# Kernel optimization log

Hardware: AMD Instinct MI355X
Metric: run time of the kernel (lower is better)

The kernel has to match this reference:

```python
import jax, jax.numpy as jnp
import numpy as np

P = 512       # person_attrs_dim
Z = 4096      # num_zones
T = 16384     # number of timesteps
E = 65536     # number of edges
PENALTY = 10.0


def setup_inputs() -> dict:
    key = jax.random.key(0)
    ks = jax.random.split(key, 10)
    person_attrs = jax.random.normal(ks[0], (P,), dtype=jnp.float32)
    times = jax.random.uniform(ks[1], (T,), dtype=jnp.float32)
    zone_features = jax.random.normal(ks[2], (Z, 16), dtype=jnp.float32)
    edge_index = jax.random.randint(ks[3], (2, E), 0, Z, dtype=jnp.int64)
    s = 0.05
    W1 = jax.random.normal(ks[4], (P + 1, 128), dtype=jnp.float32) * s
    b1 = jnp.zeros((128,), jnp.float32)
    W2 = jax.random.normal(ks[5], (128, 64), dtype=jnp.float32) * s
    b2 = jnp.zeros((64,), jnp.float32)
    W3 = jax.random.normal(ks[6], (64, Z), dtype=jnp.float32) * s
    b3 = jnp.zeros((Z,), jnp.float32)
    return {
        "person_attrs": person_attrs, "times": times,
        "zone_features": zone_features, "edge_index": edge_index,
        "W1": W1, "b1": b1, "W2": W2, "b2": b2, "W3": W3, "b3": b3,
    }


def reference(person_attrs, times, zone_features, edge_index, W1, b1, W2, b2, W3, b3):
    Zn = W3.shape[1]
    Tn = times.shape[0]

    # ---- set_graph_data: symmetric adjacency + self loops ----
    adj = jnp.zeros((Zn, Zn), jnp.float32)
    adj = adj.at[edge_index[0], edge_index[1]].set(1.0)
    adj = adj.at[edge_index[1], edge_index[0]].set(1.0)
    diag = jnp.arange(Zn)
    adj = adj.at[diag, diag].set(1.0)

    # ---- batched MLP over all timesteps (inputs don't depend on decode state) ----
    # input per step: concat(person_attrs, time)  -> [T, P+1]
    x = jnp.concatenate(
        [jnp.broadcast_to(person_attrs, (Tn, person_attrs.shape[0])), times[:, None]],
        axis=1,
    )
    h = jax.nn.relu(x @ W1 + b1)          # [T, 128]  (dropout is identity in eval)
    h = jax.nn.relu(h @ W2 + b2)          # [T, 64]
    raw = h @ W3 + b3                     # [T, Z]

    # ---- sequential graph-masked decode (training=True soft-penalty branch) ----
    def step(cur_zone, raw_t):
        constrained = raw_t - PENALTY * (1.0 - adj[cur_zone])  # [Z]
        nxt = jnp.argmax(constrained).astype(jnp.int32)
        return nxt, constrained

    _, zone_logits = jax.lax.scan(step, jnp.int32(0), raw)     # [T, Z]
    return zone_logits
```

## Files before the change

kernel.cpp:

```cpp
#include <hip/hip_runtime.h>
#include <hip/hip_bf16.h>
#include <stdint.h>

typedef uint16_t u16;
typedef uint32_t u32;
typedef uint64_t u64;
typedef unsigned char u8;

#define TT 16384
#define ZZ 4096
#define EE 65536
#define LBLK 32
#define NBLK 512
#define SUPW 16
#define NSUP 32
#define ADJ_STRIDE 80
#define UCAP 2048
#define PEN 10.0f

#define WS_BITS   0x000000
#define WS_GMKEY  0x200000
#define WS_DEG    0x220000
#define WS_ADJL   0x224000
#define WS_NCH    0x2C4000
#define WS_CVEC   0x2C5000
#define WS_WVEC   0x2C5200
#define WS_H2     0x2C5400
#define WS_M      WS_H2
#define WS_H      0x6C5400
#define WS_SB     0x705400
#define WS_CUR    0x705C00

__device__ __forceinline__ u32 sfu(float v) {
  u32 u = __float_as_uint(v);
  return u ^ ((u32)((int)u >> 31) | 0x80000000u);
}
__device__ __forceinline__ u64 mkkey(float v, u32 z) {
  return ((u64)sfu(v) << 12) | (u64)(4095u - z);
}
__device__ __forceinline__ float key_val(u64 k) {
  u32 sf = (u32)(k >> 12);
  u32 u = (sf & 0x80000000u) ? (sf ^ 0x80000000u) : ~sf;
  return __uint_as_float(u);
}

__device__ __forceinline__ u64 eval_part(int s, int part, const u32* keys, u64 gkey,
                                         const u16* adjl, int nc) {
  const u64* alq = (const u64*)(adjl + (size_t)s * ADJ_STRIDE);
  u64 c0 = (part      < nc) ? alq[part]      : 0;
  u64 c1 = (part + 4  < nc) ? alq[part + 4]  : 0;
  u64 c2 = (part + 8  < nc) ? alq[part + 8]  : 0;
  u64 c3 = (part + 12 < nc) ? alq[part + 12] : 0;
  u64 c4 = (part + 16 < nc) ? alq[part + 16] : 0;
  u64 bb = gkey;
#define CM(cv, cnd) if (cnd) {                                                   \
    u32 lo = (u32)(cv), hi = (u32)((cv) >> 32);                                  \
    u32 za = lo & 0xFFFFu, zb = lo >> 16, zc = hi & 0xFFFFu, zd = hi >> 16;      \
    u64 k0 = ((u64)keys[za] << 32) | (u64)(za ^ 0xFFFu);                         \
    u64 k1 = ((u64)keys[zb] << 32) | (u64)(zb ^ 0xFFFu);                         \
    u64 k2 = ((u64)keys[zc] << 32) | (u64)(zc ^ 0xFFFu);                         \
    u64 k3 = ((u64)keys[zd] << 32) | (u64)(zd ^ 0xFFFu);                         \
    u64 t01 = k0 > k1 ? k0 : k1; u64 t23 = k2 > k3 ? k2 : k3;                    \
    u64 tm = t01 > t23 ? t01 : t23;                                              \
    bb = tm > bb ? tm : bb; }
  CM(c0, part < nc) CM(c1, part + 4 < nc) CM(c2, part + 8 < nc)
  CM(c3, part + 12 < nc) CM(c4, part + 16 < nc)
#undef CM
  return bb;
}

__global__ __launch_bounds__(256) void k_setupA(u32* bits, u32* deg, u16* adjl,
                                                const float* pa, const float* W1,
                                                const float* b1,
                                                float* cvec, float* wvec) {
  __shared__ float pal[512];
  int tid = threadIdx.x;
  if (blockIdx.x < 16) {
    int z = blockIdx.x * 256 + tid;
    bits[(size_t)z * 128 + (z >> 5)] = 1u << (z & 31);
    deg[z] = 1;
    adjl[(size_t)z * ADJ_STRIDE] = (u16)z;
    return;
  }
  for (int i = tid; i < 512; i += 256) pal[i] = pa[i];
  __syncthreads();
  if (tid < 128) {
    float acc = b1[tid];
    for (int i = 0; i < 512; i++) acc = fmaf(pal[i], W1[(size_t)i * 128 + tid], acc);
    cvec[tid] = acc;
    wvec[tid] = W1[512 * 128 + tid];
  }
}

__global__ void k_edges(const int* ei, u32* bits, u32* deg, u16* adjl) {
  int e = blockIdx.x * blockDim.x + threadIdx.x;
  if (e >= EE) return;
  int u = ei[e], v = ei[EE + e];
#pragma unroll
  for (int dir = 0; dir < 2; dir++) {
    int a = dir ? v : u, b = dir ? u : v;
    u32 bit = 1u << (b & 31);
    u32 old = atomicOr(&bits[(size_t)a * 128 + (b >> 5)], bit);
    if (!(old & bit)) {
      u32 p = atomicAdd(&deg[a], 1u);
      if (p < ADJ_STRIDE) adjl[(size_t)a * ADJ_STRIDE + p] = (u16)b;
    }
  }
}

__global__ __launch_bounds__(256) void k_setupC(const u32* deg, u16* adjl, u8* nchp,
                                                const float* times, const float* W2,
                                                const float* b2, const float* cvec,
                                                const float* wvec, float* h2) {
  __shared__ float W2T[64][132];
  __shared__ float h1b[4][128];
  __shared__ float cl[128], wl[128], b2l[64];
  int tid = threadIdx.x;
  if (blockIdx.x < 16) {
    int z = blockIdx.x * 256 + tid;
    int d = (int)deg[z]; if (d > ADJ_STRIDE) d = ADJ_STRIDE;
    int dp = (d + 3) & ~3;
    for (int k = d; k < dp; k++) adjl[(size_t)z * ADJ_STRIDE + k] = (u16)z;
    nchp[z] = (u8)(dp >> 2);
    return;
  }
  for (int idx = tid; idx < 128 * 64; idx += 256) {
    int i = idx >> 6, j = idx & 63;
    W2T[j][i] = W2[idx];
  }
  if (tid < 128) { cl[tid] = cvec[tid]; wl[tid] = wvec[tid]; }
  else if (tid < 192) b2l[tid - 128] = b2[tid - 128];
  __syncthreads();
  int w = tid >> 6, lane = tid & 63;
  int t = (blockIdx.x - 16) * 4 + w;
  float tv = times[t];
  h1b[w][lane]      = fmaxf(fmaf(tv, wl[lane],      cl[lane]),      0.f);
  h1b[w][lane + 64] = fmaxf(fmaf(tv, wl[lane + 64], cl[lane + 64]), 0.f);
  __syncthreads();
  float acc = b2l[lane];
  const float4* hr = (const float4*)&h1b[w][0];
  const float4* Wr = (const float4*)&W2T[lane][0];
#pragma unroll
  for (int i4 = 0; i4 < 32; i4++) {
    float4 a = hr[i4], bb = Wr[i4];
    acc += a.x * bb.x; acc += a.y * bb.y; acc += a.z * bb.z; acc += a.w * bb.w;
  }
  acc = fmaxf(acc, 0.f);
  h2[(size_t)t * 64 + lane] = acc;
}

__global__ __launch_bounds__(512) void k_raw(const float* h2, const float* W3,
                                             const float* b3, float* out,
                                             u64* gmkey) {
  __shared__ float w3t[64][128];
  __shared__ float h2t[64][72];
  int tid = threadIdx.x;
  int zblk = blockIdx.x & 31, tblk = blockIdx.x >> 5;
  int z0 = zblk * 128, t0 = tblk * 64;
#pragma unroll
  for (int it = 0; it < 4; it++) {
    int f4 = tid + it * 512;
    int k = f4 >> 5, jj = (f4 & 31) * 4;
    *(float4*)&w3t[k][jj] = *(const float4*)(W3 + (size_t)k * ZZ + z0 + jj);
  }
#pragma unroll
  for (int it = 0; it < 2; it++) {
    int f4 = tid + it * 512;
    int r = f4 >> 4, kk = (f4 & 15) * 4;
    float4 h = *(const float4*)(h2 + (size_t)(t0 + r) * 64 + kk);
    h2t[kk + 0][r] = h.x; h2t[kk + 1][r] = h.y;
    h2t[kk + 2][r] = h.z; h2t[kk + 3][r] = h.w;
  }
  __syncthreads();
  int zq = tid & 31, tq = tid >> 5;
  float4 acc[4];
#pragma unroll
  for (int r = 0; r < 4; r++) acc[r] = make_float4(0.f, 0.f, 0.f, 0.f);
  for (int k = 0; k < 64; k++) {
    float4 w = *(const float4*)&w3t[k][zq * 4];
    float4 h = *(const float4*)&h2t[k][tq * 4];
    acc[0].x += h.x * w.x; acc[0].y += h.x * w.y; acc[0].z += h.x * w.z; acc[0].w += h.x * w.w;
    acc[1].x += h.y * w.x; acc[1].y += h.y * w.y; acc[1].z += h.y * w.z; acc[1].w += h.y * w.w;
    acc[2].x += h.z * w.x; acc[2].y += h.z * w.y; acc[2].z += h.z * w.z; acc[2].w += h.z * w.w;
    acc[3].x += h.w * w.x; acc[3].y += h.w * w.y; acc[3].z += h.w * w.z; acc[3].w += h.w * w.w;
  }
  int z = z0 + zq * 4;
  float4 b3v = *(const float4*)(b3 + z);
  int lane = tid & 63;
  int half = lane >> 5;
#pragma unroll
  for (int r = 0; r < 4; r++) {
    int t = t0 + tq * 4 + r;
    float4 v;
    v.x = acc[r].x + b3v.x - PEN; v.y = acc[r].y + b3v.y - PEN;
    v.z = acc[r].z + b3v.z - PEN; v.w = acc[r].w + b3v.w - PEN;
    *(float4*)(out + (size_t)t * ZZ + z) = v;
    float lv = v.x; u32 lz = (u32)z;
    if (v.y > lv) { lv = v.y; lz = (u32)(z + 1); }
    if (v.z > lv) { lv = v.z; lz = (u32)(z + 2); }
    if (v.w > lv) { lv = v.w; lz = (u32)(z + 3); }
    float mv = lv;
#pragma unroll
    for (int off = 16; off >= 1; off >>= 1) {
      float o = __shfl_xor(mv, off);
      mv = o > mv ? o : mv;
    }
    u64 msk = __ballot(lv == mv);
    u32 hm = (u32)(msk >> (half * 32));
    int fl = __ffs(hm) - 1 + half * 32;
    u32 zbest = __shfl(lz, fl);
    if ((lane & 31) == 0)
      atomicMax((unsigned long long*)&gmkey[t], (unsigned long long)mkkey(mv, zbest));
  }
}

__global__ __launch_bounds__(512) void k_stage1(const float* raw, const u16* adjl,
                                                const u8* nchp, const u64* gmkey,
                                                u16* M) {
  __shared__ u32 keys[ZZ];
  __shared__ u16 ev0[ZZ];
  __shared__ u16 ev[ZZ];
  __shared__ u16 R[ZZ];
  __shared__ u16 U0[UCAP];
  __shared__ u16 U[2][UCAP];
  __shared__ u8  nchl[ZZ];
  __shared__ u32 markw[128];
  __shared__ u32 mcnt2[2];
  __shared__ u64 gmk[LBLK];
  int tid = threadIdx.x;
  int b = blockIdx.x, t0 = b * LBLK;
  *(u64*)&nchl[tid * 8] = *(const u64*)(nchp + tid * 8);
  if (tid < LBLK) gmk[tid] = gmkey[t0 + tid];
  {
    const float4* src = (const float4*)(raw + (size_t)t0 * ZZ);
    float4 r0 = src[tid], r1 = src[tid + 512];
    ((uint4*)keys)[tid]       = make_uint4(sfu(r0.x), sfu(r0.y), sfu(r0.z), sfu(r0.w));
    ((uint4*)keys)[tid + 512] = make_uint4(sfu(r1.x), sfu(r1.y), sfu(r1.z), sfu(r1.w));
  }
  if (tid < 128) markw[tid] = 0;
  if (tid == 128) { mcnt2[0] = 0; mcnt2[1] = 0; }
  __syncthreads();
  int lane = tid & 63;
  u64 lmask = (((u64)1) << lane) - 1ull;
  int part = tid & 3;
  {
    const float4* srcn = (const float4*)(raw + (size_t)(t0 + 1) * ZZ);
    float4 p0 = srcn[tid], p1 = srcn[tid + 512];
    u64 gk = gmk[0];
    float gv = key_val(gk) - PEN;
    u64 gkey = ((u64)sfu(gv) << 32) | (u64)(gk & 0xFFFu);
    for (int u = tid; u < ZZ * 4; u += 512) {
      int s = u >> 2;
      u64 pk = eval_part(s, part, keys, gkey, adjl, (int)nchl[s]);
      u64 o1 = __shfl_xor(pk, 1); pk = o1 > pk ? o1 : pk;
      u64 o2 = __shfl_xor(pk, 2); pk = o2 > pk ? o2 : pk;
      if (part == 0) ev0[s] = (u16)(4095u - ((u32)pk & 0xFFFu));
    }
    __syncthreads();
    for (int ch = 0; ch < 8; ch++) {
      u32 ns = ev0[ch * 512 + tid];
      u32 wi = ns >> 5, bit = 1u << (ns & 31);
      u32 old = atomicOr(&markw[wi], bit);
      bool isnew = !(old & bit);
      u64 msk = __ballot(isnew ? 1 : 0);
      u32 base = 0;
      if (lane == 0) base = msk ? atomicAdd(&mcnt2[0], (u32)__popcll(msk)) : 0u;
      base = __shfl(base, 0);
      if (isnew) {
        u32 idx = base + (u32)__popcll(msk & lmask);
        if (idx < UCAP) { U[0][idx] = (u16)ns; U0[idx] = (u16)ns; }
        R[ns] = (u16)ns;
      }
    }
    ((uint4*)keys)[tid]       = make_uint4(sfu(p0.x), sfu(p0.y), sfu(p0.z), sfu(p0.w));
    ((uint4*)keys)[tid + 512] = make_uint4(sfu(p1.x), sfu(p1.y), sfu(p1.z), sfu(p1.w));
    __syncthreads();
  }
  int m0r = (int)mcnt2[0];
  bool full0 = (m0r > UCAP);
  int m0 = full0 ? ZZ : m0r;
  if (full0) {
#pragma unroll
    for (int q = 0; q < 8; q++) {
      int j = tid + q * 512;
      R[j] = (u16)j;
    }
    __syncthreads();
  }
  int m = m0;
  bool dense = full0;
  int pb = 0;
  for (int i = 1; i < LBLK; i++) {
    int t = t0 + i;
    int tn = t + 1; if (tn > TT - 1) tn = TT - 1;
    const float4* srcn = (const float4*)(raw + (size_t)tn * ZZ);
    float4 p0 = srcn[tid], p1 = srcn[tid + 512];
    if (tid < 128) markw[tid] = 0;
    if (tid == 128) mcnt2[pb ^ 1] = 0;
    u64 gk = gmk[i];
    float gv = key_val(gk) - PEN;
    u64 gkey = ((u64)sfu(gv) << 32) | (u64)(gk & 0xFFFu);
    int m4 = m << 2;
    for (int u = tid; u < m4; u += 512) {
      int s = dense ? (u >> 2) : (int)U[pb][u >> 2];
      u64 pk = eval_part(s, part, keys, gkey, adjl, (int)nchl[s]);
      u64 o1 = __shfl_xor(pk, 1); pk = o1 > pk ? o1 : pk;
      u64 o2 = __shfl_xor(pk, 2); pk = o2 > pk ? o2 : pk;
      if (part == 0) ev[s] = (u16)(4095u - ((u32)pk & 0xFFFu));
    }
    __syncthreads();
    for (int u = tid; u < m0; u += 512) {
      int v = full0 ? u : (int)U0[u];
      R[v] = ev[R[v]];
    }
    for (int u = tid; u < m; u += 512) {
      int s = dense ? u : (int)U[pb][u];
      u32 ns = ev[s];
      u32 wi = ns >> 5, bit = 1u << (ns & 31);
      u32 old = atomicOr(&markw[wi], bit);
      bool isnew = !(old & bit);
      u64 msk = __ballot(isnew ? 1 : 0);
      u32 base = 0;
      if (lane == 0) base = msk ? atomicAdd(&mcnt2[pb ^ 1], (u32)__popcll(msk)) : 0u;
      base = __shfl(base, 0);
      if (isnew) {
        u32 idx = base + (u32)__popcll(msk & lmask);
        if (idx < UCAP) U[pb ^ 1][idx] = (u16)ns;
      }
    }
    ((uint4*)keys)[tid]       = make_uint4(sfu(p0.x), sfu(p0.y), sfu(p0.z), sfu(p0.w));
    ((uint4*)keys)[tid + 512] = make_uint4(sfu(p1.x), sfu(p1.y), sfu(p1.z), sfu(p1.w));
    __syncthreads();
    m = (int)mcnt2[pb ^ 1];
    dense = (m > UCAP);
    if (dense) m = ZZ;
    pb ^= 1;
  }
  {
    int j0 = tid * 8;
    u64 w0 = (u64)R[ev0[j0 + 0]]
           | ((u64)R[ev0[j0 + 1]] << 16)
           | ((u64)R[ev0[j0 + 2]] << 32)
           | ((u64)R[ev0[j0 + 3]] << 48);
    u64 w1 = (u64)R[ev0[j0 + 4]]
           | ((u64)R[ev0[j0 + 5]] << 16)
           | ((u64)R[ev0[j0 + 6]] << 32)
           | ((u64)R[ev0[j0 + 7]] << 48);
    u64* md = (u64*)(M + (size_t)b * ZZ);
    md[tid * 2]     = w0;
    md[tid * 2 + 1] = w1;
  }
}

__global__ __launch_bounds__(256) void k_super(const u16* G, u16* H) {
  int g = blockIdx.x, tid = threadIdx.x;
  u32 v[16];
#pragma unroll
  for (int q = 0; q < 16; q++) v[q] = G[(size_t)(g * SUPW) * ZZ + tid + q * 256];
  for (int k = 1; k < SUPW; k++) {
    const u16* Gk = G + (size_t)(g * SUPW + k) * ZZ;
#pragma unroll
    for (int q = 0; q < 16; q++) v[q] = Gk[v[q]];
  }
#pragma unroll
  for (int q = 0; q < 16; q++) H[(size_t)g * ZZ + tid + q * 256] = (u16)v[q];
}

__global__ void k_chase(const u16* G, const u16* H, u32* sb) {
  __shared__ u32 ug[NSUP];
  int tid = threadIdx.x;
  if (tid == 0) {
    u32 s = 0;
    for (int g = 0; g < NSUP; g++) { ug[g] = s; s = H[(size_t)g * ZZ + s]; }
  }
  __syncthreads();
  if (tid < NSUP) {
    u32 s = ug[tid];
    for (int k = 0; k < SUPW; k++) {
      int b = tid * SUPW + k;
      sb[b] = s;
      s = G[(size_t)b * ZZ + s];
    }
  }
}

__global__ __launch_bounds__(64) void k_replay2(const float* out, const u16* adjl,
                                                const u8* nchp, const u64* gmkey,
                                                const u32* sb, u32* curz) {
  int b = blockIdx.x, t0 = b * LBLK;
  int lane = threadIdx.x;
  u32 s = sb[b];
  for (int i = 0; i < LBLK; i++) {
    int t = t0 + i;
    if (lane == 0) curz[t] = s;
    u64 gk = gmkey[t];
    float gv = key_val(gk) - PEN;
    u32 gi = 4095u - (u32)(gk & 0xFFFu);
    int dp = ((int)nchp[s]) << 2;
    const u16* al = adjl + (size_t)s * ADJ_STRIDE;
    const float* r = out + (size_t)t * ZZ;
    float bv = gv; u32 bi = gi;
    if (lane < dp) {
      u32 nb = al[lane]; float v = r[nb];
      if (v > bv || (v == bv && nb < bi)) { bv = v; bi = nb; }
    }
    if (lane + 64 < dp) {
      u32 nb = al[lane + 64]; float v = r[nb];
      if (v > bv || (v == bv && nb < bi)) { bv = v; bi = nb; }
    }
#pragma unroll
    for (int off = 32; off >= 1; off >>= 1) {
      float ov = __shfl_xor(bv, off);
      u32 oi  = __shfl_xor(bi, off);
      if (ov > bv || (ov == bv && oi < bi)) { bv = ov; bi = oi; }
    }
    s = bi;
  }
}

__global__ __launch_bounds__(256) void k_out2(float* out, const u32* curz, const u32* bits) {
  int t = blockIdx.x * 4 + (threadIdx.x >> 6);
  int lane = threadIdx.x & 63;
  u32 c = curz[t];
  u64 w = ((const u64*)(bits + (size_t)c * 128))[lane];
  float* p = out + (size_t)t * ZZ + lane * 64;
  while (w) {
    int bpos = __ffsll((unsigned long long)w) - 1;
    p[bpos] += PEN;
    w &= w - 1;
  }
}

extern "C" void kernel_launch(void* const* d_in, const int* in_sizes, int n_in,
                              void* d_out, int out_size, void* d_ws, size_t ws_size,
                              hipStream_t stream) {
  const float* pa    = (const float*)d_in[0];
  const float* times = (const float*)d_in[1];
  const int*   ei    = (const int*)d_in[3];
  const float* W1    = (const float*)d_in[4];
  const float* b1    = (const float*)d_in[5];
  const float* W2    = (const float*)d_in[6];
  const float* b2    = (const float*)d_in[7];
  const float* W3    = (const float*)d_in[8];
  const float* b3    = (const float*)d_in[9];
  float* out = (float*)d_out;
  char* ws = (char*)d_ws;

  u32* bits = (u32*)(ws + WS_BITS);
  u64* gmkey = (u64*)(ws + WS_GMKEY);
  u32* deg  = (u32*)(ws + WS_DEG);
  u16* adjl = (u16*)(ws + WS_ADJL);
  u8*  nchp = (u8*)(ws + WS_NCH);
  float* cvec = (float*)(ws + WS_CVEC);
  float* wvec = (float*)(ws + WS_WVEC);
  float* h2   = (float*)(ws + WS_H2);
  u16* M = (u16*)(ws + WS_M);
  u16* H = (u16*)(ws + WS_H);
  u32* sb   = (u32*)(ws + WS_SB);
  u32* curz = (u32*)(ws + WS_CUR);

  hipMemsetAsync(ws, 0, 0x220000, stream);
  hipLaunchKernelGGL(k_setupA, dim3(17), dim3(256), 0, stream,
                     bits, deg, adjl, pa, W1, b1, cvec, wvec);
  hipLaunchKernelGGL(k_edges, dim3(EE / 256), dim3(256), 0, stream, ei, bits, deg, adjl);
  hipLaunchKernelGGL(k_setupC, dim3(16 + TT / 4), dim3(256), 0, stream,
                     deg, adjl, nchp, times, W2, b2, cvec, wvec, h2);
  hipLaunchKernelGGL(k_raw, dim3(8192), dim3(512), 0, stream, h2, W3, b3, out, gmkey);
  hipLaunchKernelGGL(k_stage1, dim3(NBLK), dim3(512), 0, stream, out, adjl, nchp, gmkey, M);
  hipLaunchKernelGGL(k_super, dim3(NSUP), dim3(256), 0, stream, M, H);
  hipLaunchKernelGGL(k_chase, dim3(1), dim3(64), 0, stream, M, H, sb);
  hipLaunchKernelGGL(k_replay2, dim3(NBLK), dim3(64), 0, stream, out, adjl, nchp, gmkey, sb, curz);
  hipLaunchKernelGGL(k_out2, dim3(TT / 4), dim3(256), 0, stream, out, curz, bits);
}
```

Measured before the change: 411.1 us.

## Track per-source paths instead of dedup frontier in stage1 decode composition

The sparse path of stage1 drops the per-step frontier deduplication (atomicOr marks, ballot compaction, double-buffered U lists). It instead advances each of the m0 initial unique states independently through all 32 steps, writing results in place in S. Keys are double-buffered, so each step needs one barrier instead of two. The dense fallback recomputes all states and composes R each step. This removes atomics and barriers but forgoes merging paths that converge, and UCAP is halved so the dense fallback triggers more often.

```diff
diff --git a/kernel.cpp b/kernel.cpp
--- a/kernel.cpp
+++ b/kernel.cpp
@@ -15,7 +15,7 @@
 #define SUPW 16
 #define NSUP 32
 #define ADJ_STRIDE 80
-#define UCAP 2048
+#define UCAP 1024
 #define PEN 10.0f
 
 #define WS_BITS   0x000000
@@ -217,15 +217,15 @@
 __global__ __launch_bounds__(512) void k_stage1(const float* raw, const u16* adjl,
                                                 const u8* nchp, const u64* gmkey,
                                                 u16* M) {
-  __shared__ u32 keys[ZZ];
+  __shared__ u32 keys[2][ZZ];
   __shared__ u16 ev0[ZZ];
-  __shared__ u16 ev[ZZ];
   __shared__ u16 R[ZZ];
+  __shared__ u16 evf[ZZ];
   __shared__ u16 U0[UCAP];
-  __shared__ u16 U[2][UCAP];
+  __shared__ u16 S[UCAP];
   __shared__ u8  nchl[ZZ];
   __shared__ u32 markw[128];
-  __shared__ u32 mcnt2[2];
+  __shared__ u32 mcnt;
   __shared__ u64 gmk[LBLK];
   int tid = threadIdx.x;
   int b = blockIdx.x, t0 = b * LBLK;
@@ -234,11 +234,11 @@
   {
     const float4* src = (const float4*)(raw + (size_t)t0 * ZZ);
     float4 r0 = src[tid], r1 = src[tid + 512];
-    ((uint4*)keys)[tid]       = make_uint4(sfu(r0.x), sfu(r0.y), sfu(r0.z), sfu(r0.w));
-    ((uint4*)keys)[tid + 512] = make_uint4(sfu(r1.x), sfu(r1.y), sfu(r1.z), sfu(r1.w));
+    ((uint4*)keys[0])[tid]       = make_uint4(sfu(r0.x), sfu(r0.y), sfu(r0.z), sfu(r0.w));
+    ((uint4*)keys[0])[tid + 512] = make_uint4(sfu(r1.x), sfu(r1.y), sfu(r1.z), sfu(r1.w));
   }
   if (tid < 128) markw[tid] = 0;
-  if (tid == 128) { mcnt2[0] = 0; mcnt2[1] = 0; }
+  if (tid == 128) mcnt = 0;
   __syncthreads();
   int lane = tid & 63;
   u64 lmask = (((u64)1) << lane) - 1ull;
@@ -251,7 +251,7 @@
     u64 gkey = ((u64)sfu(gv) << 32) | (u64)(gk & 0xFFFu);
     for (int u = tid; u < ZZ * 4; u += 512) {
       int s = u >> 2;
-      u64 pk = eval_part(s, part, keys, gkey, adjl, (int)nchl[s]);
+      u64 pk = eval_part(s, part, keys[0], gkey, adjl, (int)nchl[s]);
       u64 o1 = __shfl_xor(pk, 1); pk = o1 > pk ? o1 : pk;
       u64 o2 = __shfl_xor(pk, 2); pk = o2 > pk ? o2 : pk;
       if (part == 0) ev0[s] = (u16)(4095u - ((u32)pk & 0xFFFu));
@@ -264,77 +264,71 @@
       bool isnew = !(old & bit);
       u64 msk = __ballot(isnew ? 1 : 0);
       u32 base = 0;
-      if (lane == 0) base = msk ? atomicAdd(&mcnt2[0], (u32)__popcll(msk)) : 0u;
+      if (lane == 0) base = msk ? atomicAdd(&mcnt, (u32)__popcll(msk)) : 0u;
       base = __shfl(base, 0);
       if (isnew) {
         u32 idx = base + (u32)__popcll(msk & lmask);
-        if (idx < UCAP) { U[0][idx] = (u16)ns; U0[idx] = (u16)ns; }
-        R[ns] = (u16)ns;
+        if (idx < UCAP) { U0[idx] = (u16)ns; S[idx] = (u16)ns; }
       }
     }
-    ((uint4*)keys)[tid]       = make_uint4(sfu(p0.x), sfu(p0.y), sfu(p0.z), sfu(p0.w));
-    ((uint4*)keys)[tid + 512] = make_uint4(sfu(p1.x), sfu(p1.y), sfu(p1.z), sfu(p1.w));
+    ((uint4*)keys[1])[tid]       = make_uint4(sfu(p0.x), sfu(p0.y), sfu(p0.z), sfu(p0.w));
+    ((uint4*)keys[1])[tid + 512] = make_uint4(sfu(p1.x), sfu(p1.y), sfu(p1.z), sfu(p1.w));
     __syncthreads();
   }
-  int m0r = (int)mcnt2[0];
-  bool full0 = (m0r > UCAP);
-  int m0 = full0 ? ZZ : m0r;
-  if (full0) {
-#pragma unroll
-    for (int q = 0; q < 8; q++) {
-      int j = tid + q * 512;
-      R[j] = (u16)j;
-    }
+  int m0 = (int)mcnt;
+  int cur = 1;
+  if (m0 <= UCAP) {
+    for (int i = 1; i < LBLK; i++) {
+      int tn = t0 + i + 1; if (tn > TT - 1) tn = TT - 1;
+      const float4* srcn = (const float4*)(raw + (size_t)tn * ZZ);
+      float4 p0 = srcn[tid], p1 = srcn[tid + 512];
+      u64 gk = gmk[i];
+      float gv = key_val(gk) - PEN;
+      u64 gkey = ((u64)sfu(gv) << 32) | (u64)(gk & 0xFFFu);
+      const u32* kc = keys[cur];
+      for (int u = tid >> 2; u < m0; u += 128) {
+        int s = (int)S[u];
+        u64 pk = eval_part(s, part, kc, gkey, adjl, (int)nchl[s]);
+        u64 o1 = __shfl_xor(pk, 1); pk = o1 > pk ? o1 : pk;
+        u64 o2 = __shfl_xor(pk, 2); pk = o2 > pk ? o2 : pk;
+        if (part == 0) S[u] = (u16)(4095u - ((u32)pk & 0xFFFu));
+      }
+      u32* kn = keys[cur ^ 1];
+      ((uint4*)kn)[tid]       = make_uint4(sfu(p0.x), sfu(p0.y), sfu(p0.z), sfu(p0.w));
+      ((uint4*)kn)[tid + 512] = make_uint4(sfu(p1.x), sfu(p1.y), sfu(p1.z), sfu(p1.w));
+      __syncthreads();
+      cur ^= 1;
+    }
+    for (int u = tid; u < m0; u += 512) R[U0[u]] = S[u];
     __syncthreads();
-  }
-  int m = m0;
-  bool dense = full0;
-  int pb = 0;
-  for (int i = 1; i < LBLK; i++) {
-    int t = t0 + i;
-    int tn = t + 1; if (tn > TT - 1) tn = TT - 1;
-    const float4* srcn = (const float4*)(raw + (size_t)tn * ZZ);
-    float4 p0 = srcn[tid], p1 = srcn[tid + 512];
-    if (tid < 128) markw[tid] = 0;
-    if (tid == 128) mcnt2[pb ^ 1] = 0;
-    u64 gk = gmk[i];
-    float gv = key_val(gk) - PEN;
-    u64 gkey = ((u64)sfu(gv) << 32) | (u64)(gk & 0xFFFu);
-    int m4 = m << 2;
-    for (int u = tid; u < m4; u += 512) {
-      int s = dense ? (u >> 2) : (int)U[pb][u >> 2];
-      u64 pk = eval_part(s, part, keys, gkey, adjl, (int)nchl[s]);
-      u64 o1 = __shfl_xor(pk, 1); pk = o1 > pk ? o1 : pk;
-      u64 o2 = __shfl_xor(pk, 2); pk = o2 > pk ? o2 : pk;
-      if (part == 0) ev[s] = (u16)(4095u - ((u32)pk & 0xFFFu));
-    }
+  } else {
+#pragma unroll
+    for (int q = 0; q < 8; q++) { int j = tid + q * 512; R[j] = (u16)j; }
     __syncthreads();
-    for (int u = tid; u < m0; u += 512) {
-      int v = full0 ? u : (int)U0[u];
-      R[v] = ev[R[v]];
-    }
-    for (int u = tid; u < m; u += 512) {
-      int s = dense ? u : (int)U[pb][u];
-      u32 ns = ev[s];
-      u32 wi = ns >> 5, bit = 1u << (ns & 31);
-      u32 old = atomicOr(&markw[wi], bit);
-      bool isnew = !(old & bit);
-      u64 msk = __ballot(isnew ? 1 : 0);
-      u32 base = 0;
-      if (lane == 0) base = msk ? atomicAdd(&mcnt2[pb ^ 1], (u32)__popcll(msk)) : 0u;
-      base = __shfl(base, 0);
-      if (isnew) {
-        u32 idx = base + (u32)__popcll(msk & lmask);
-        if (idx < UCAP) U[pb ^ 1][idx] = (u16)ns;
+    for (int i = 1; i < LBLK; i++) {
+      int tn = t0 + i + 1; if (tn > TT - 1) tn = TT - 1;
+      const float4* srcn = (const float4*)(raw + (size_t)tn * ZZ);
+      float4 p0 = srcn[tid], p1 = srcn[tid + 512];
+      u64 gk = gmk[i];
+      float gv = key_val(gk) - PEN;
+      u64 gkey = ((u64)sfu(gv) << 32) | (u64)(gk & 0xFFFu);
+      const u32* kc = keys[cur];
+      for (int u = tid; u < ZZ * 4; u += 512) {
+        int s = u >> 2;
+        u64 pk = eval_part(s, part, kc, gkey, adjl, (int)nchl[s]);
+        u64 o1 = __shfl_xor(pk, 1); pk = o1 > pk ? o1 : pk;
+        u64 o2 = __shfl_xor(pk, 2); pk = o2 > pk ? o2 : pk;
+        if (part == 0) evf[s] = (u16)(4095u - ((u32)pk & 0xFFFu));
       }
-    }
-    ((uint4*)keys)[tid]       = make_uint4(sfu(p0.x), sfu(p0.y), sfu(p0.z), sfu(p0.w));
-    ((uint4*)keys)[tid + 512] = make_uint4(sfu(p1.x), sfu(p1.y), sfu(p1.z), sfu(p1.w));
-    __syncthreads();
-    m = (int)mcnt2[pb ^ 1];
-    dense = (m > UCAP);
-    if (dense) m = ZZ;
-    pb ^= 1;
+      __syncthreads();
+#pragma unroll
+      for (int q = 0; q < 8; q++) { int j = tid + q * 512; R[j] = evf[R[j]]; }
+      u32* kn = keys[cur ^ 1];
+      ((uint4*)kn)[tid]       = make_uint4(sfu(p0.x), sfu(p0.y), sfu(p0.z), sfu(p0.w));
+      ((uint4*)kn)[tid + 512] = make_uint4(sfu(p1.x), sfu(p1.y), sfu(p1.z), sfu(p1.w));
+      __syncthreads();
+      cur ^= 1;
+    }
   }
   {
     int j0 = tid * 8;
```

After: 468.5 us. 14.0% more time.
